# Optimization experiments

Measured on AMD Instinct MI355X. Metric: run time of the kernel, lower is better.

## Reference

```python
import jax, jax.numpy as jnp
import numpy as np

N_NODES = 50000
N_EDGES = 500000
IN_DIM = 256
HEADS = 4
OUT_C = 64
NEG_SLOPE = 0.2


def setup_inputs() -> dict:
    key = jax.random.key(0)
    ks = jax.random.split(key, 6)
    x = jax.random.normal(ks[0], (N_NODES, IN_DIM), dtype=jnp.float32)
    edge_index = jax.random.randint(ks[1], (2, N_EDGES), 0, N_NODES, dtype=jnp.int64)
    scale = 1.0 / np.sqrt(IN_DIM)
    W_l = jax.random.normal(ks[2], (IN_DIM, HEADS * OUT_C), dtype=jnp.float32) * scale
    W_r = jax.random.normal(ks[3], (IN_DIM, HEADS * OUT_C), dtype=jnp.float32) * scale
    b_l = jnp.zeros((HEADS * OUT_C,), dtype=jnp.float32)
    b_r = jnp.zeros((HEADS * OUT_C,), dtype=jnp.float32)
    att = jax.random.normal(ks[4], (HEADS, OUT_C), dtype=jnp.float32) * (1.0 / np.sqrt(OUT_C))
    bias = jnp.zeros((HEADS * OUT_C,), dtype=jnp.float32)
    return {"x": x, "edge_index": edge_index, "W_l": W_l, "b_l": b_l,
            "W_r": W_r, "b_r": b_r, "att": att, "bias": bias}


def _gatv2(x, edge_index, W_l, b_l, W_r, b_r, att, bias):
    N = x.shape[0]
    H, C = att.shape
    # add self loops (PyG GATv2Conv default add_self_loops=True)
    loop = jnp.arange(N, dtype=edge_index.dtype)
    src = jnp.concatenate([edge_index[0], loop])  # message sources (x_j)
    dst = jnp.concatenate([edge_index[1], loop])  # aggregation targets (x_i)
    x_l = (x @ W_l + b_l).reshape(N, H, C)  # source-side projection
    x_r = (x @ W_r + b_r).reshape(N, H, C)  # target-side projection
    # GATv2 attention logits: a^T LeakyReLU(x_l[src] + x_r[dst])
    e = jax.nn.leaky_relu(x_l[src] + x_r[dst], NEG_SLOPE)  # [E, H, C]
    logits = jnp.einsum('ehc,hc->eh', e, att)              # [E, H]
    # segmented softmax over incoming edges of each dst node
    m = jax.ops.segment_max(logits, dst, num_segments=N)   # [N, H]
    ex = jnp.exp(logits - m[dst])
    denom = jax.ops.segment_sum(ex, dst, num_segments=N)   # [N, H]
    alpha = ex / denom[dst]                                # [E, H]
    # weighted scatter-aggregation of source messages
    out = jax.ops.segment_sum(x_l[src] * alpha[:, :, None], dst, num_segments=N)  # [N, H, C]
    return out.reshape(N, H * C) + bias


def reference(x, edge_index, W_l, b_l, W_r, b_r, att, bias):
    out = _gatv2(x, edge_index, W_l, b_l, W_r, b_r, att, bias)  # [N, H*C]
    # wrapper: single relation -> reshape(-1, 1, output_dim) and cat on dim=1
    return out.reshape(-1, 1, HEADS * OUT_C)
```

## Files before the change

kernel.cpp:

```cpp
#include <hip/hip_runtime.h>
#include <hip/hip_bf16.h>
#include <math.h>

#define N_NODES 50000
#define N_PAD   50048
#define N_EDGES 500000
#define E_TOT   550000
#define HC      256
#define NHC     512
#define HEADS   4
#define NEG     0.2f

typedef __attribute__((ext_vector_type(8))) short short8;
typedef __attribute__((ext_vector_type(4))) float f32x4;

__device__ __forceinline__ ushort f2bf(float f) {
    union { float f; unsigned u; } c; c.f = f;
    unsigned u = c.u;
    unsigned rounded = u + 0x7FFFu + ((u >> 16) & 1u);
    return (ushort)(rounded >> 16);
}
__device__ __forceinline__ float bf2f(ushort u) {
    return __uint_as_float((unsigned)u << 16);
}

static constexpr size_t OFF_COUNTS = 0;
static constexpr size_t OFF_ROWS   = OFF_COUNTS + (size_t)N_NODES * 4;
static constexpr size_t OFF_CUR    = OFF_ROWS + (size_t)(N_NODES + 1) * 4;
static constexpr size_t OFF_SRCS   = OFF_CUR + (size_t)N_NODES * 4;
static constexpr size_t OFF_BSUM   = OFF_SRCS + (size_t)E_TOT * 4;
static constexpr size_t OFF_MODE   = OFF_BSUM + 64 * 4;
static constexpr size_t OFF_XB     = ((OFF_MODE + 4 + 255) / 256) * 256;
static constexpr size_t OFF_WT     = OFF_XB + (size_t)N_PAD * HC * 2;
static constexpr size_t OFF_XLB    = OFF_WT + (size_t)NHC * HC * 2;
static constexpr size_t OFF_XRB    = OFF_XLB + (size_t)N_NODES * HC * 2;

__device__ __forceinline__ int get_src(const int* __restrict__ ei, int mode, int e) {
    if (e >= N_EDGES) return e - N_EDGES;
    return mode ? ei[2 * e] : ei[e];
}
__device__ __forceinline__ int get_dst(const int* __restrict__ ei, int mode, int e) {
    if (e >= N_EDGES) return e - N_EDGES;
    return mode ? ei[2 * (N_EDGES + e)] : ei[N_EDGES + e];
}

__global__ void detect_kernel(const int* __restrict__ ei, int* __restrict__ mode) {
    __shared__ int any;
    if (threadIdx.x == 0) any = 0;
    __syncthreads();
    if (ei[2 * threadIdx.x + 1] != 0) atomicOr(&any, 1);
    __syncthreads();
    if (threadIdx.x == 0) mode[0] = (any == 0) ? 1 : 0;
}

__global__ __launch_bounds__(256) void cvt_x_kernel(const float* __restrict__ x,
                                                    ushort* __restrict__ xb) {
    size_t i = ((size_t)blockIdx.x * 256 + threadIdx.x) * 8;
    if (i >= (size_t)N_PAD * HC) return;
    ushort o[8];
    if (i < (size_t)N_NODES * HC) {
        float4 v0 = *(const float4*)(x + i);
        float4 v1 = *(const float4*)(x + i + 4);
        o[0] = f2bf(v0.x); o[1] = f2bf(v0.y); o[2] = f2bf(v0.z); o[3] = f2bf(v0.w);
        o[4] = f2bf(v1.x); o[5] = f2bf(v1.y); o[6] = f2bf(v1.z); o[7] = f2bf(v1.w);
    } else {
#pragma unroll
        for (int j = 0; j < 8; ++j) o[j] = 0;
    }
    *(short8*)(xb + i) = *(short8*)o;
}

__global__ __launch_bounds__(256) void cvt_w_kernel(const float* __restrict__ Wl,
                                                    const float* __restrict__ Wr,
                                                    ushort* __restrict__ wt) {
    int i = blockIdx.x * 256 + threadIdx.x;
    if (i >= NHC * HC) return;
    int n = i >> 8, k = i & 255;
    float v = (n < HC) ? Wl[(size_t)k * HC + n] : Wr[(size_t)k * HC + (n - HC)];
    wt[i] = f2bf(v);
}

#define BM 128
#define BK 32
__global__ __launch_bounds__(256) void mfma_gemm_kernel(
        const __hip_bfloat16* __restrict__ xb, const __hip_bfloat16* __restrict__ wt,
        const float* __restrict__ bl, const float* __restrict__ br,
        ushort* __restrict__ xlb, ushort* __restrict__ xrb) {
    __shared__ __hip_bfloat16 As[2][BM * BK];
    __shared__ __hip_bfloat16 Bs[2][BM * BK];
    const int t    = threadIdx.x;
    const int lane = t & 63;
    const int wid  = t >> 6;
    const int wr   = wid >> 1, wc = wid & 1;
    const int brow = blockIdx.x * BM;
    const int bcol = blockIdx.y * BM;

    auto stage = [&](int buf, int k0) {
#pragma unroll
        for (int r = 0; r < 2; ++r) {
            int c = r * 256 + t;
            const __hip_bfloat16* ga = xb + ((size_t)(brow + (c >> 2)) * HC + k0 + (c & 3) * 8);
            __builtin_amdgcn_global_load_lds(
                (const __attribute__((address_space(1))) void*)ga,
                (__attribute__((address_space(3))) void*)((char*)&As[buf][0] + c * 16),
                16, 0, 0);
        }
#pragma unroll
        for (int r = 0; r < 2; ++r) {
            int c = r * 256 + t;
            const __hip_bfloat16* gb = wt + ((size_t)(bcol + (c >> 2)) * HC + k0 + (c & 3) * 8);
            __builtin_amdgcn_global_load_lds(
                (const __attribute__((address_space(1))) void*)gb,
                (__attribute__((address_space(3))) void*)((char*)&Bs[buf][0] + c * 16),
                16, 0, 0);
        }
    };

    f32x4 acc[4][4];
#pragma unroll
    for (int m = 0; m < 4; ++m)
#pragma unroll
        for (int n = 0; n < 4; ++n) acc[m][n] = (f32x4)0.f;

    stage(0, 0);
    __syncthreads();

    const int rsub = lane & 15;
    const int koff = (lane >> 4) * 16;

    for (int kk = 0; kk < 8; ++kk) {
        const int cur = kk & 1;
        if (kk < 7) stage(cur ^ 1, (kk + 1) * BK);
        short8 a[4], b[4];
#pragma unroll
        for (int m = 0; m < 4; ++m)
            a[m] = *(const short8*)((const char*)&As[cur][0] +
                    (wr * 64 + m * 16 + rsub) * (BK * 2) + koff);
#pragma unroll
        for (int n = 0; n < 4; ++n)
            b[n] = *(const short8*)((const char*)&Bs[cur][0] +
                    (wc * 64 + n * 16 + rsub) * (BK * 2) + koff);
#pragma unroll
        for (int m = 0; m < 4; ++m)
#pragma unroll
            for (int n = 0; n < 4; ++n)
                acc[m][n] = __builtin_amdgcn_mfma_f32_16x16x32_bf16(a[m], b[n], acc[m][n], 0, 0, 0);
        __syncthreads();
    }

    ushort* dst = (bcol < HC) ? xlb : xrb;
    const float* bvec = (bcol < HC) ? bl : br;
    const int cb = bcol & (HC - 1);
#pragma unroll
    for (int m = 0; m < 4; ++m) {
#pragma unroll
        for (int n = 0; n < 4; ++n) {
            int col = cb + wc * 64 + n * 16 + (lane & 15);
            float bv = bvec[col];
#pragma unroll
            for (int j = 0; j < 4; ++j) {
                int row = brow + wr * 64 + m * 16 + (lane >> 4) * 4 + j;
                if (row < N_NODES) dst[(size_t)row * HC + col] = f2bf(acc[m][n][j] + bv);
            }
        }
    }
}

__global__ void count_kernel(const int* __restrict__ ei, const int* __restrict__ mode,
                             int* __restrict__ counts) {
    int e = blockIdx.x * blockDim.x + threadIdx.x;
    if (e < E_TOT) atomicAdd(&counts[get_dst(ei, *mode, e)], 1);
}

__global__ void scan1_kernel(const int* __restrict__ counts, int* __restrict__ rows,
                             int* __restrict__ bsum) {
    __shared__ int sdata[256];
    const int t = threadIdx.x;
    const int base = blockIdx.x * 1024 + t * 4;
    int v[4]; int s = 0;
#pragma unroll
    for (int j = 0; j < 4; ++j) {
        int idx = base + j;
        v[j] = (idx < N_NODES) ? counts[idx] : 0;
        s += v[j];
    }
    sdata[t] = s;
    __syncthreads();
    for (int off = 1; off < 256; off <<= 1) {
        int xv = (t >= off) ? sdata[t - off] : 0;
        __syncthreads();
        sdata[t] += xv;
        __syncthreads();
    }
    int run = sdata[t] - s;
#pragma unroll
    for (int j = 0; j < 4; ++j) {
        int idx = base + j;
        if (idx < N_NODES) rows[idx] = run;
        run += v[j];
    }
    if (t == 255) bsum[blockIdx.x] = sdata[255];
}

__global__ void scan2_kernel(int* __restrict__ bsum, int* __restrict__ rows) {
    if (threadIdx.x == 0 && blockIdx.x == 0) {
        int run = 0;
        for (int b = 0; b < 49; ++b) { int xv = bsum[b]; bsum[b] = run; run += xv; }
        rows[N_NODES] = E_TOT;
    }
}

__global__ void scan3_kernel(int* __restrict__ rows, const int* __restrict__ bsum) {
    int idx = blockIdx.x * 256 + threadIdx.x;
    if (idx < N_NODES) rows[idx] += bsum[idx >> 10];
}

__global__ void fill_kernel(const int* __restrict__ ei, const int* __restrict__ mode,
                            const int* __restrict__ rows, int* __restrict__ cursor,
                            int* __restrict__ srcs) {
    int e = blockIdx.x * blockDim.x + threadIdx.x;
    if (e < E_TOT) {
        int md = *mode;
        int d = get_dst(ei, md, e);
        int s = get_src(ei, md, e);
        int pos = atomicAdd(&cursor[d], 1);
        srcs[rows[d] + pos] = s;
    }
}

__global__ __launch_bounds__(256) void fused_agg_kernel(
        const ushort* __restrict__ xlb, const ushort* __restrict__ xrb,
        const float* __restrict__ att,
        const int* __restrict__ rows, const int* __restrict__ srcs,
        const float* __restrict__ bias, float* __restrict__ out) {
    const int lane = threadIdx.x & 63;
    const int n = (blockIdx.x * 256 + threadIdx.x) >> 6;
    if (n >= N_NODES) return;
    const int half = lane >> 5;
    const int sl   = lane & 31;
    const int start = rows[n], end = rows[n + 1];

    float xr[8], at[8];
    {
        union { uint4 v; ushort u[8]; } c;
        c.v = *(const uint4*)(xrb + (size_t)n * HC + sl * 8);
#pragma unroll
        for (int j = 0; j < 8; ++j) xr[j] = bf2f(c.u[j]);
        float4 a0 = *(const float4*)&att[sl * 8];
        float4 a1 = *(const float4*)&att[sl * 8 + 4];
        at[0] = a0.x; at[1] = a0.y; at[2] = a0.z; at[3] = a0.w;
        at[4] = a1.x; at[5] = a1.y; at[6] = a1.z; at[7] = a1.w;
    }

    float sm = 0.f;
    float acc[8];
#pragma unroll
    for (int j = 0; j < 8; ++j) acc[j] = 0.f;

    int i = start + half;
    uint4 row_nxt = make_uint4(0, 0, 0, 0);
    if (i < end) row_nxt = *(const uint4*)(xlb + (size_t)srcs[i] * HC + sl * 8);

    for (; i < end; i += 2) {
        union { uint4 v; ushort u[8]; } c;
        c.v = row_nxt;
        if (i + 2 < end)
            row_nxt = *(const uint4*)(xlb + (size_t)srcs[i + 2] * HC + sl * 8);

        float xv[8];
#pragma unroll
        for (int j = 0; j < 8; ++j) xv[j] = bf2f(c.u[j]);

        float p = 0.f;
#pragma unroll
        for (int j = 0; j < 8; ++j) {
            float v = xv[j] + xr[j];
            v = fmaxf(v, NEG * v);
            p = fmaf(v, at[j], p);
        }
        p += __shfl_xor(p, 1, 64);
        p += __shfl_xor(p, 2, 64);
        p += __shfl_xor(p, 4, 64);

        float w = __expf(p);
        sm += w;
#pragma unroll
        for (int j = 0; j < 8; ++j) acc[j] = fmaf(w, xv[j], acc[j]);
    }

    sm += __shfl_xor(sm, 32, 64);
#pragma unroll
    for (int j = 0; j < 8; ++j) acc[j] += __shfl_xor(acc[j], 32, 64);

    if (half == 0) {
        const float inv = 1.0f / sm;
        float4 b0 = *(const float4*)&bias[sl * 8];
        float4 b1 = *(const float4*)&bias[sl * 8 + 4];
        float4 o0, o1;
        o0.x = fmaf(acc[0], inv, b0.x); o0.y = fmaf(acc[1], inv, b0.y);
        o0.z = fmaf(acc[2], inv, b0.z); o0.w = fmaf(acc[3], inv, b0.w);
        o1.x = fmaf(acc[4], inv, b1.x); o1.y = fmaf(acc[5], inv, b1.y);
        o1.z = fmaf(acc[6], inv, b1.z); o1.w = fmaf(acc[7], inv, b1.w);
        *(float4*)&out[(size_t)n * HC + sl * 8]     = o0;
        *(float4*)&out[(size_t)n * HC + sl * 8 + 4] = o1;
    }
}

extern "C" void kernel_launch(void* const* d_in, const int* in_sizes, int n_in,
                              void* d_out, int out_size, void* d_ws, size_t ws_size,
                              hipStream_t stream) {
    const float* x    = (const float*)d_in[0];
    const int*   ei   = (const int*)d_in[1];
    const float* Wl   = (const float*)d_in[2];
    const float* bl   = (const float*)d_in[3];
    const float* Wr   = (const float*)d_in[4];
    const float* br   = (const float*)d_in[5];
    const float* att  = (const float*)d_in[6];
    const float* bias = (const float*)d_in[7];
    float* out = (float*)d_out;

    char* ws = (char*)d_ws;
    int*   counts = (int*)(ws + OFF_COUNTS);
    int*   rows   = (int*)(ws + OFF_ROWS);
    int*   cursor = (int*)(ws + OFF_CUR);
    int*   srcs   = (int*)(ws + OFF_SRCS);
    int*   bsum   = (int*)(ws + OFF_BSUM);
    int*   mode   = (int*)(ws + OFF_MODE);
    ushort* xb    = (ushort*)(ws + OFF_XB);
    ushort* wt    = (ushort*)(ws + OFF_WT);
    ushort* xlb   = (ushort*)(ws + OFF_XLB);
    ushort* xrb   = (ushort*)(ws + OFF_XRB);

    (void)hipMemsetAsync(counts, 0, (size_t)N_NODES * 4, stream);
    (void)hipMemsetAsync(cursor, 0, (size_t)N_NODES * 4, stream);

    detect_kernel<<<1, 256, 0, stream>>>(ei, mode);

    cvt_x_kernel<<<(int)(((size_t)N_PAD * HC / 8 + 255) / 256), 256, 0, stream>>>(x, xb);
    cvt_w_kernel<<<(NHC * HC + 255) / 256, 256, 0, stream>>>(Wl, Wr, wt);

    dim3 ggrid(N_PAD / BM, NHC / BM);
    mfma_gemm_kernel<<<ggrid, 256, 0, stream>>>(
        (const __hip_bfloat16*)xb, (const __hip_bfloat16*)wt, bl, br, xlb, xrb);

    count_kernel<<<(E_TOT + 255) / 256, 256, 0, stream>>>(ei, mode, counts);
    scan1_kernel<<<49, 256, 0, stream>>>(counts, rows, bsum);
    scan2_kernel<<<1, 64, 0, stream>>>(bsum, rows);
    scan3_kernel<<<(N_NODES + 255) / 256, 256, 0, stream>>>(rows, bsum);
    fill_kernel<<<(E_TOT + 255) / 256, 256, 0, stream>>>(ei, mode, rows, cursor, srcs);

    fused_agg_kernel<<<(N_NODES + 3) / 4, 256, 0, stream>>>(
        xlb, xrb, att, rows, srcs, bias, out);
}
```

Before: 182.8 us.

## Merge scan kernels and memsets, pack f32x2 math and prefetch indices in aggregation

Replaces the three-kernel prefix scan with one 1024-thread single-block scan, and moves cursor next to counts so a single memset clears both. This cuts launch count and memset overhead. The aggregation kernel now uses packed two-wide float math with cheaper bf16 unpacking so the compiler can emit packed FP32 instructions. It also prefetches the source index two iterations ahead to shorten the dependent load chain. The single-block scan is serial per thread (about 49 elements each) and may be slow.

```diff
diff --git a/kernel.cpp b/kernel.cpp
--- a/kernel.cpp
+++ b/kernel.cpp
@@ -13,6 +13,7 @@
 
 typedef __attribute__((ext_vector_type(8))) short short8;
 typedef __attribute__((ext_vector_type(4))) float f32x4;
+typedef __attribute__((ext_vector_type(2))) float f32x2;
 
 __device__ __forceinline__ ushort f2bf(float f) {
     union { float f; unsigned u; } c; c.f = f;
@@ -20,16 +21,12 @@
     unsigned rounded = u + 0x7FFFu + ((u >> 16) & 1u);
     return (ushort)(rounded >> 16);
 }
-__device__ __forceinline__ float bf2f(ushort u) {
-    return __uint_as_float((unsigned)u << 16);
-}
 
 static constexpr size_t OFF_COUNTS = 0;
-static constexpr size_t OFF_ROWS   = OFF_COUNTS + (size_t)N_NODES * 4;
-static constexpr size_t OFF_CUR    = OFF_ROWS + (size_t)(N_NODES + 1) * 4;
-static constexpr size_t OFF_SRCS   = OFF_CUR + (size_t)N_NODES * 4;
-static constexpr size_t OFF_BSUM   = OFF_SRCS + (size_t)E_TOT * 4;
-static constexpr size_t OFF_MODE   = OFF_BSUM + 64 * 4;
+static constexpr size_t OFF_CUR    = OFF_COUNTS + (size_t)N_NODES * 4;
+static constexpr size_t OFF_ROWS   = OFF_CUR + (size_t)N_NODES * 4;
+static constexpr size_t OFF_SRCS   = OFF_ROWS + (size_t)(N_NODES + 1) * 4;
+static constexpr size_t OFF_MODE   = OFF_SRCS + (size_t)E_TOT * 4;
 static constexpr size_t OFF_XB     = ((OFF_MODE + 4 + 255) / 256) * 256;
 static constexpr size_t OFF_WT     = OFF_XB + (size_t)N_PAD * HC * 2;
 static constexpr size_t OFF_XLB    = OFF_WT + (size_t)NHC * HC * 2;
@@ -172,47 +169,32 @@
     if (e < E_TOT) atomicAdd(&counts[get_dst(ei, *mode, e)], 1);
 }
 
-__global__ void scan1_kernel(const int* __restrict__ counts, int* __restrict__ rows,
-                             int* __restrict__ bsum) {
-    __shared__ int sdata[256];
+#define SCAN_T 1024
+__global__ __launch_bounds__(SCAN_T) void scan_kernel(const int* __restrict__ counts,
+                                                      int* __restrict__ rows) {
+    __shared__ int part[SCAN_T];
     const int t = threadIdx.x;
-    const int base = blockIdx.x * 1024 + t * 4;
-    int v[4]; int s = 0;
-#pragma unroll
-    for (int j = 0; j < 4; ++j) {
+    const int per = (N_NODES + SCAN_T - 1) / SCAN_T;
+    const int base = t * per;
+    int s = 0;
+    for (int j = 0; j < per; ++j) {
         int idx = base + j;
-        v[j] = (idx < N_NODES) ? counts[idx] : 0;
-        s += v[j];
-    }
-    sdata[t] = s;
+        if (idx < N_NODES) s += counts[idx];
+    }
+    part[t] = s;
     __syncthreads();
-    for (int off = 1; off < 256; off <<= 1) {
-        int xv = (t >= off) ? sdata[t - off] : 0;
+    for (int off = 1; off < SCAN_T; off <<= 1) {
+        int v = (t >= off) ? part[t - off] : 0;
         __syncthreads();
-        sdata[t] += xv;
+        part[t] += v;
         __syncthreads();
     }
-    int run = sdata[t] - s;
-#pragma unroll
-    for (int j = 0; j < 4; ++j) {
+    int run = part[t] - s;
+    for (int j = 0; j < per; ++j) {
         int idx = base + j;
-        if (idx < N_NODES) rows[idx] = run;
-        run += v[j];
-    }
-    if (t == 255) bsum[blockIdx.x] = sdata[255];
-}
-
-__global__ void scan2_kernel(int* __restrict__ bsum, int* __restrict__ rows) {
-    if (threadIdx.x == 0 && blockIdx.x == 0) {
-        int run = 0;
-        for (int b = 0; b < 49; ++b) { int xv = bsum[b]; bsum[b] = run; run += xv; }
-        rows[N_NODES] = E_TOT;
-    }
-}
-
-__global__ void scan3_kernel(int* __restrict__ rows, const int* __restrict__ bsum) {
-    int idx = blockIdx.x * 256 + threadIdx.x;
-    if (idx < N_NODES) rows[idx] += bsum[idx >> 10];
+        if (idx < N_NODES) { rows[idx] = run; run += counts[idx]; }
+    }
+    if (t == 0) rows[N_NODES] = E_TOT;
 }
 
 __global__ void fill_kernel(const int* __restrict__ ei, const int* __restrict__ mode,
@@ -240,67 +222,80 @@
     const int sl   = lane & 31;
     const int start = rows[n], end = rows[n + 1];
 
-    float xr[8], at[8];
+    f32x2 xr2[4], at2[4];
     {
-        union { uint4 v; ushort u[8]; } c;
-        c.v = *(const uint4*)(xrb + (size_t)n * HC + sl * 8);
-#pragma unroll
-        for (int j = 0; j < 8; ++j) xr[j] = bf2f(c.u[j]);
+        uint4 c = *(const uint4*)(xrb + (size_t)n * HC + sl * 8);
+        unsigned w[4] = {c.x, c.y, c.z, c.w};
+#pragma unroll
+        for (int j = 0; j < 4; ++j) {
+            xr2[j][0] = __uint_as_float(w[j] << 16);
+            xr2[j][1] = __uint_as_float(w[j] & 0xffff0000u);
+        }
         float4 a0 = *(const float4*)&att[sl * 8];
         float4 a1 = *(const float4*)&att[sl * 8 + 4];
-        at[0] = a0.x; at[1] = a0.y; at[2] = a0.z; at[3] = a0.w;
-        at[4] = a1.x; at[5] = a1.y; at[6] = a1.z; at[7] = a1.w;
-    }
-
+        at2[0][0] = a0.x; at2[0][1] = a0.y; at2[1][0] = a0.z; at2[1][1] = a0.w;
+        at2[2][0] = a1.x; at2[2][1] = a1.y; at2[3][0] = a1.z; at2[3][1] = a1.w;
+    }
+
+    f32x2 acc2[4];
+#pragma unroll
+    for (int j = 0; j < 4; ++j) acc2[j] = (f32x2)0.f;
     float sm = 0.f;
-    float acc[8];
-#pragma unroll
-    for (int j = 0; j < 8; ++j) acc[j] = 0.f;
 
     int i = start + half;
-    uint4 row_nxt = make_uint4(0, 0, 0, 0);
-    if (i < end) row_nxt = *(const uint4*)(xlb + (size_t)srcs[i] * HC + sl * 8);
+    uint4 rA = make_uint4(0, 0, 0, 0);
+    int sB = -1;
+    if (i < end) rA = *(const uint4*)(xlb + (size_t)srcs[i] * HC + sl * 8);
+    if (i + 2 < end) sB = srcs[i + 2];
 
     for (; i < end; i += 2) {
-        union { uint4 v; ushort u[8]; } c;
-        c.v = row_nxt;
-        if (i + 2 < end)
-            row_nxt = *(const uint4*)(xlb + (size_t)srcs[i + 2] * HC + sl * 8);
-
-        float xv[8];
-#pragma unroll
-        for (int j = 0; j < 8; ++j) xv[j] = bf2f(c.u[j]);
-
-        float p = 0.f;
-#pragma unroll
-        for (int j = 0; j < 8; ++j) {
-            float v = xv[j] + xr[j];
-            v = fmaxf(v, NEG * v);
-            p = fmaf(v, at[j], p);
-        }
+        uint4 r = rA;
+        if (sB >= 0) rA = *(const uint4*)(xlb + (size_t)sB * HC + sl * 8);
+        sB = (i + 4 < end) ? srcs[i + 4] : -1;
+
+        unsigned w[4] = {r.x, r.y, r.z, r.w};
+        f32x2 xv[4];
+#pragma unroll
+        for (int j = 0; j < 4; ++j) {
+            xv[j][0] = __uint_as_float(w[j] << 16);
+            xv[j][1] = __uint_as_float(w[j] & 0xffff0000u);
+        }
+
+        f32x2 p2 = (f32x2)0.f;
+#pragma unroll
+        for (int j = 0; j < 4; ++j) {
+            f32x2 v = xv[j] + xr2[j];
+            f32x2 lk = __builtin_elementwise_max(v, v * NEG);
+            p2 = lk * at2[j] + p2;
+        }
+        float p = p2[0] + p2[1];
         p += __shfl_xor(p, 1, 64);
         p += __shfl_xor(p, 2, 64);
         p += __shfl_xor(p, 4, 64);
 
-        float w = __expf(p);
-        sm += w;
-#pragma unroll
-        for (int j = 0; j < 8; ++j) acc[j] = fmaf(w, xv[j], acc[j]);
+        float wgt = __expf(p);
+        sm += wgt;
+        f32x2 w2; w2[0] = wgt; w2[1] = wgt;
+#pragma unroll
+        for (int j = 0; j < 4; ++j) acc2[j] = xv[j] * w2 + acc2[j];
     }
 
     sm += __shfl_xor(sm, 32, 64);
 #pragma unroll
-    for (int j = 0; j < 8; ++j) acc[j] += __shfl_xor(acc[j], 32, 64);
+    for (int j = 0; j < 4; ++j) {
+        acc2[j][0] += __shfl_xor(acc2[j][0], 32, 64);
+        acc2[j][1] += __shfl_xor(acc2[j][1], 32, 64);
+    }
 
     if (half == 0) {
         const float inv = 1.0f / sm;
         float4 b0 = *(const float4*)&bias[sl * 8];
         float4 b1 = *(const float4*)&bias[sl * 8 + 4];
         float4 o0, o1;
-        o0.x = fmaf(acc[0], inv, b0.x); o0.y = fmaf(acc[1], inv, b0.y);
-        o0.z = fmaf(acc[2], inv, b0.z); o0.w = fmaf(acc[3], inv, b0.w);
-        o1.x = fmaf(acc[4], inv, b1.x); o1.y = fmaf(acc[5], inv, b1.y);
-        o1.z = fmaf(acc[6], inv, b1.z); o1.w = fmaf(acc[7], inv, b1.w);
+        o0.x = fmaf(acc2[0][0], inv, b0.x); o0.y = fmaf(acc2[0][1], inv, b0.y);
+        o0.z = fmaf(acc2[1][0], inv, b0.z); o0.w = fmaf(acc2[1][1], inv, b0.w);
+        o1.x = fmaf(acc2[2][0], inv, b1.x); o1.y = fmaf(acc2[2][1], inv, b1.y);
+        o1.z = fmaf(acc2[3][0], inv, b1.z); o1.w = fmaf(acc2[3][1], inv, b1.w);
         *(float4*)&out[(size_t)n * HC + sl * 8]     = o0;
         *(float4*)&out[(size_t)n * HC + sl * 8 + 4] = o1;
     }
@@ -321,18 +316,16 @@
 
     char* ws = (char*)d_ws;
     int*   counts = (int*)(ws + OFF_COUNTS);
+    int*   cursor = (int*)(ws + OFF_CUR);
     int*   rows   = (int*)(ws + OFF_ROWS);
-    int*   cursor = (int*)(ws + OFF_CUR);
     int*   srcs   = (int*)(ws + OFF_SRCS);
-    int*   bsum   = (int*)(ws + OFF_BSUM);
     int*   mode   = (int*)(ws + OFF_MODE);
     ushort* xb    = (ushort*)(ws + OFF_XB);
     ushort* wt    = (ushort*)(ws + OFF_WT);
     ushort* xlb   = (ushort*)(ws + OFF_XLB);
     ushort* xrb   = (ushort*)(ws + OFF_XRB);
 
-    (void)hipMemsetAsync(counts, 0, (size_t)N_NODES * 4, stream);
-    (void)hipMemsetAsync(cursor, 0, (size_t)N_NODES * 4, stream);
+    (void)hipMemsetAsync(counts, 0, (size_t)N_NODES * 8, stream);
 
     detect_kernel<<<1, 256, 0, stream>>>(ei, mode);
 
@@ -344,9 +337,7 @@
         (const __hip_bfloat16*)xb, (const __hip_bfloat16*)wt, bl, br, xlb, xrb);
 
     count_kernel<<<(E_TOT + 255) / 256, 256, 0, stream>>>(ei, mode, counts);
-    scan1_kernel<<<49, 256, 0, stream>>>(counts, rows, bsum);
-    scan2_kernel<<<1, 64, 0, stream>>>(bsum, rows);
-    scan3_kernel<<<(N_NODES + 255) / 256, 256, 0, stream>>>(rows, bsum);
+    scan_kernel<<<1, SCAN_T, 0, stream>>>(counts, rows);
     fill_kernel<<<(E_TOT + 255) / 256, 256, 0, stream>>>(ei, mode, rows, cursor, srcs);
 
     fused_agg_kernel<<<(N_NODES + 3) / 4, 256, 0, stream>>>(
```

New measurement: 256.5 us. +40.3%, slower.
